# Kernel tuning notes

Hardware: AMD Instinct MI355X
Metric: run time of the kernel (lower is better)

## Reference

```python
import jax, jax.numpy as jnp
import numpy as np

N_NODES = 20000
N_EDGES = 160000
N_GRAPHS = 1000
IN_DIM = 11
HID = 128
EDGE_DIM = 3
N_LAYERS = 5
BN_EPS = 1e-5


def setup_inputs() -> dict:
    key = jax.random.key(0)
    ks = jax.random.split(key, 24)
    x = jax.random.normal(ks[0], (N_NODES, IN_DIM), dtype=jnp.float32)
    edge_index = jax.random.randint(ks[1], (2, N_EDGES), 0, N_NODES, dtype=jnp.int64)
    batch = jnp.sort(jax.random.randint(ks[2], (N_NODES,), 0, N_GRAPHS, dtype=jnp.int64))
    edge_attr = jax.random.uniform(ks[3], (N_EDGES, EDGE_DIM), dtype=jnp.float32)
    s_in = 1.0 / np.sqrt(IN_DIM)
    s_z = 1.0 / np.sqrt(2 * HID + EDGE_DIM)
    s_h = 1.0 / np.sqrt(HID)
    W_in = jax.random.uniform(ks[4], (IN_DIM, HID), minval=-s_in, maxval=s_in)
    b_in = jax.random.uniform(ks[5], (HID,), minval=-s_in, maxval=s_in)
    Wf = jax.random.uniform(ks[6], (N_LAYERS, 2 * HID + EDGE_DIM, HID), minval=-s_z, maxval=s_z)
    bf = jax.random.uniform(ks[7], (N_LAYERS, HID), minval=-s_z, maxval=s_z)
    Ws = jax.random.uniform(ks[8], (N_LAYERS, 2 * HID + EDGE_DIM, HID), minval=-s_z, maxval=s_z)
    bs = jax.random.uniform(ks[9], (N_LAYERS, HID), minval=-s_z, maxval=s_z)
    gamma = jnp.ones((N_LAYERS, HID), dtype=jnp.float32)
    beta = jnp.zeros((N_LAYERS, HID), dtype=jnp.float32)
    W1 = jax.random.uniform(ks[10], (HID, HID), minval=-s_h, maxval=s_h)
    b1 = jax.random.uniform(ks[11], (HID,), minval=-s_h, maxval=s_h)
    W2 = jax.random.uniform(ks[12], (HID, HID), minval=-s_h, maxval=s_h)
    b2 = jax.random.uniform(ks[13], (HID,), minval=-s_h, maxval=s_h)
    W3 = jax.random.uniform(ks[14], (HID, 1), minval=-s_h, maxval=s_h)
    b3 = jax.random.uniform(ks[15], (1,), minval=-s_h, maxval=s_h)
    return {"x": x, "edge_index": edge_index, "batch": batch, "edge_attr": edge_attr,
            "W_in": W_in, "b_in": b_in, "Wf": Wf, "bf": bf, "Ws": Ws, "bs": bs,
            "gamma": gamma, "beta": beta, "W1": W1, "b1": b1, "W2": W2, "b2": b2,
            "W3": W3, "b3": b3}


def reference(x, edge_index, batch, edge_attr, W_in, b_in, Wf, bf, Ws, bs,
              gamma, beta, W1, b1, W2, b2, W3, b3):
    src = edge_index[0]  # x_j (source / neighbor)
    dst = edge_index[1]  # x_i (target / aggregation index)
    # in-degree per node for mean aggregation (zero-degree -> divide by 1, yields 0)
    deg = jax.ops.segment_sum(jnp.ones((N_EDGES,), jnp.float32), dst, num_segments=N_NODES)
    deg = jnp.maximum(deg, 1.0)[:, None]

    h = x @ W_in + b_in  # [N, H]
    for l in range(N_LAYERS):
        # CGConv: z = [x_i, x_j, e]; msg = sigmoid(z Wf) * softplus(z Ws); residual + mean-aggr
        z = jnp.concatenate([h[dst], h[src], edge_attr], axis=-1)  # [E, 2H+D]
        msg = jax.nn.sigmoid(z @ Wf[l] + bf[l]) * jax.nn.softplus(z @ Ws[l] + bs[l])
        agg = jax.ops.segment_sum(msg, dst, num_segments=N_NODES) / deg
        h = h + agg
        # BatchNorm1d (training-mode batch stats, biased variance)
        mu = jnp.mean(h, axis=0)
        var = jnp.mean((h - mu) ** 2, axis=0)
        h = (h - mu) * jax.lax.rsqrt(var + BN_EPS) * gamma[l] + beta[l]
        h = jax.nn.relu(h)
        # dropout omitted (eval mode)

    # global mean pool over graphs
    cnt = jax.ops.segment_sum(jnp.ones((N_NODES,), jnp.float32), batch, num_segments=N_GRAPHS)
    g = jax.ops.segment_sum(h, batch, num_segments=N_GRAPHS) / jnp.maximum(cnt, 1.0)[:, None]

    g = jax.nn.relu(g @ W1 + b1)
    g = jax.nn.relu(g @ W2 + b2)
    return g @ W3 + b3  # [G, 1]
```

## Files before the change

kernel.cpp:

```cpp
#include <hip/hip_runtime.h>
#include <math.h>

#define NN 20000
#define NE 160000
#define NG 1000
#define IND 11
#define H 128
#define ED 3
#define NL 5
#define ZDH (259*128)
#define BN_EPSF 1e-5f
#define BPAD 17
#define EPW 16

typedef unsigned short ushort_t;
typedef unsigned int uint_t;
typedef __attribute__((ext_vector_type(8))) short bf8_t;
typedef __attribute__((ext_vector_type(4))) float f4_t;

__device__ inline ushort_t f2bf(float x) {
    unsigned int u = __float_as_uint(x);
    unsigned int r = (u + 0x7fffu + ((u >> 16) & 1u)) >> 16;
    return (ushort_t)r;
}
__device__ inline float bf2f(ushort_t b) {
    return __uint_as_float(((unsigned int)b) << 16);
}


__global__ void deg_int_kernel(const int* __restrict__ dst, int* __restrict__ degi) {
    int e = blockIdx.x * blockDim.x + threadIdx.x;
    if (e < NE) atomicAdd(&degi[dst[e]], 1);
}

__global__ __launch_bounds__(256) void reserve_kernel(const int* __restrict__ degi,
                                                      int* __restrict__ cursor,
                                                      float* __restrict__ invdeg,
                                                      int* __restrict__ counter) {
    int n = blockIdx.x * blockDim.x + threadIdx.x;
    int lane = threadIdx.x & 63;
    int v = (n < NN) ? degi[n] : 0;
    int x = v;
#pragma unroll
    for (int st = 1; st < 64; st <<= 1) {
        int y = __shfl_up(x, st, 64);
        if (lane >= st) x += y;
    }
    int total = __shfl(x, 63, 64);
    int base = 0;
    if (lane == 63) base = atomicAdd(counter, total);
    base = __shfl(base, 63, 64);
    if (n < NN) {
        cursor[n] = base + x - v;
        invdeg[n] = 1.0f / (float)(v < 1 ? 1 : v);
    }
}

__global__ void scatter_kernel(const int* __restrict__ src, const int* __restrict__ dst,
                               const float* __restrict__ ea,
                               const float* __restrict__ invdeg,
                               int* __restrict__ cursor, float4* __restrict__ csr_ea4,
                               int* __restrict__ csr_dst, float* __restrict__ csr_inv) {
    int e = blockIdx.x * blockDim.x + threadIdx.x;
    if (e < NE) {
        int d = dst[e];
        int pos = atomicAdd(&cursor[d], 1);
        float4 r;
        r.x = ea[e * ED + 0];
        r.y = ea[e * ED + 1];
        r.z = ea[e * ED + 2];
        r.w = __int_as_float(src[e]);
        csr_ea4[pos] = r;
        csr_dst[pos] = d;
        csr_inv[pos] = invdeg[d];
    }
}

__global__ void flag_kernel(const int* __restrict__ csr_dst, unsigned* __restrict__ endmask) {
    int e = blockIdx.x * blockDim.x + threadIdx.x;
    if (e < NE) {
        int d = csr_dst[e];
        int dn = (e + 1 < NE) ? csr_dst[e + 1] : -1;
        if (d != dn) atomicOr(&endmask[e >> 5], 1u << (e & 31));
    }
}

__global__ void wprep_kernel(const float* __restrict__ Wf, const float* __restrict__ Ws,
                             ushort_t* __restrict__ Wt) {
    int idx = blockIdx.x * 256 + threadIdx.x;
    if (idx >= NL * 512 * H) return;
    int k = idx & 127;
    int n = (idx >> 7) & 511;
    int l = idx >> 16;
    int t = n >> 7, j = n & 127;
    const float* W = (t == 0 || t == 2) ? Wf : Ws;
    int krow = (t < 2) ? k : (H + k);
    Wt[idx] = f2bf(W[(size_t)l * ZDH + krow * H + j]);
}


__global__ __launch_bounds__(H) void hin_kernel(const float* __restrict__ x,
                                                const float* __restrict__ Win,
                                                const float* __restrict__ bin,
                                                float* __restrict__ h) {
    int n = blockIdx.x;
    int j = threadIdx.x;
    __shared__ float xr[IND];
    if (j < IND) xr[j] = x[n * IND + j];
    __syncthreads();
    float acc = bin[j];
#pragma unroll
    for (int k = 0; k < IND; ++k) acc = fmaf(xr[k], Win[k * H + j], acc);
    h[(size_t)n * H + j] = acc;
}

__global__ __launch_bounds__(256, 2) void node_gemm_mfma(const float* __restrict__ hsrc,
                                                         float* __restrict__ hbn,
                                                         const ushort_t* __restrict__ Wt,
                                                         const float* __restrict__ sum,
                                                         const float* __restrict__ sumsq,
                                                         const float* __restrict__ gamma,
                                                         const float* __restrict__ beta,
                                                         int applyBN,
                                                         uint_t* __restrict__ ppack,
                                                         uint_t* __restrict__ qpack) {
    __shared__ __align__(16) ushort_t lbF[128 * BPAD * 8];
    __shared__ __align__(16) ushort_t lbS[128 * BPAD * 8];
    int pair = blockIdx.y;
    int wave = threadIdx.x >> 6;
    int lane = threadIdx.x & 63;
    int sub = lane & 15;
    int quad = lane >> 4;
    int m0 = blockIdx.x * 64 + wave * 16;
    int writeH = applyBN && (pair == 0);

    const ushort_t* whF = Wt + (size_t)(2 * pair) * 128 * H;
    const ushort_t* whS = Wt + (size_t)(2 * pair + 1) * 128 * H;

    for (int c = threadIdx.x; c < 2048; c += 256) {
        int n = c >> 4, k = c & 15;
        *(bf8_t*)(lbF + ((size_t)n * BPAD + k) * 8) = *(const bf8_t*)(whF + n * H + k * 8);
        *(bf8_t*)(lbS + ((size_t)n * BPAD + k) * 8) = *(const bf8_t*)(whS + n * H + k * 8);
    }

    bf8_t aHi[4], aLo[4];
    int r = m0 + sub;
    int rc = r < NN ? r : NN - 1;
#pragma unroll
    for (int ks = 0; ks < 4; ++ks) {
        int kb = ks * 32 + quad * 8;
        const float* hp = hsrc + (size_t)rc * H + kb;
        float4 v0 = *(const float4*)hp;
        float4 v1 = *(const float4*)(hp + 4);
        float vv[8] = {v0.x, v0.y, v0.z, v0.w, v1.x, v1.y, v1.z, v1.w};
        if (applyBN) {
            float4 su0 = *(const float4*)&sum[kb],   su1 = *(const float4*)&sum[kb + 4];
            float4 sq0 = *(const float4*)&sumsq[kb], sq1 = *(const float4*)&sumsq[kb + 4];
            float4 ga0 = *(const float4*)&gamma[kb], ga1 = *(const float4*)&gamma[kb + 4];
            float4 be0 = *(const float4*)&beta[kb],  be1 = *(const float4*)&beta[kb + 4];
            float su[8] = {su0.x, su0.y, su0.z, su0.w, su1.x, su1.y, su1.z, su1.w};
            float sq[8] = {sq0.x, sq0.y, sq0.z, sq0.w, sq1.x, sq1.y, sq1.z, sq1.w};
            float ga[8] = {ga0.x, ga0.y, ga0.z, ga0.w, ga1.x, ga1.y, ga1.z, ga1.w};
            float be[8] = {be0.x, be0.y, be0.z, be0.w, be1.x, be1.y, be1.z, be1.w};
#pragma unroll
            for (int i = 0; i < 8; ++i) {
                float mu  = su[i] * (1.0f / NN);
                float var = sq[i] * (1.0f / NN) - mu * mu;
                float sc  = ga[i] * rsqrtf(var + BN_EPSF);
                float sh  = be[i] - mu * sc;
                float v = fmaf(vv[i], sc, sh);
                vv[i] = v > 0.0f ? v : 0.0f;
            }
        }
        bf8_t hi8, lo8;
#pragma unroll
        for (int i = 0; i < 8; ++i) {
            ushort_t hi = f2bf(vv[i]);
            hi8[i] = (short)hi;
            lo8[i] = (short)f2bf(vv[i] - bf2f(hi));
        }
        aHi[ks] = hi8;
        aLo[ks] = lo8;
        if (writeH && r < NN) {
            float* op = hbn + (size_t)r * H + kb;
            *(float4*)op = make_float4(vv[0], vv[1], vv[2], vv[3]);
            *(float4*)(op + 4) = make_float4(vv[4], vv[5], vv[6], vv[7]);
        }
    }
    __syncthreads();

    f4_t accF[8], accS[8];
#pragma unroll
    for (int b = 0; b < 8; ++b) { accF[b] = (f4_t){0.f, 0.f, 0.f, 0.f}; accS[b] = (f4_t){0.f, 0.f, 0.f, 0.f}; }

#pragma unroll
    for (int nt = 0; nt < 8; ++nt) {
#pragma unroll
        for (int ks = 0; ks < 4; ++ks) {
            size_t lo = ((size_t)(nt * 16 + sub) * BPAD + ks * 4 + quad) * 8;
            bf8_t bF = *(const bf8_t*)(lbF + lo);
            bf8_t bS = *(const bf8_t*)(lbS + lo);
            accF[nt] = __builtin_amdgcn_mfma_f32_16x16x32_bf16(aHi[ks], bF, accF[nt], 0, 0, 0);
            accF[nt] = __builtin_amdgcn_mfma_f32_16x16x32_bf16(aLo[ks], bF, accF[nt], 0, 0, 0);
            accS[nt] = __builtin_amdgcn_mfma_f32_16x16x32_bf16(aHi[ks], bS, accS[nt], 0, 0, 0);
            accS[nt] = __builtin_amdgcn_mfma_f32_16x16x32_bf16(aLo[ks], bS, accS[nt], 0, 0, 0);
        }
    }

    uint_t* outp = pair ? qpack : ppack;
#pragma unroll
    for (int nt = 0; nt < 8; ++nt) {
        int col = nt * 16 + sub;
#pragma unroll
        for (int rr = 0; rr < 4; ++rr) {
            int row = m0 + quad * 4 + rr;
            if (row < NN) {
                uint_t lo = f2bf(accF[nt][rr]);
                uint_t hi = f2bf(accS[nt][rr]);
                outp[(size_t)row * H + col] = lo | (hi << 16);
            }
        }
    }
}

__global__ __launch_bounds__(256) void agg_edge_kernel(const int4* __restrict__ csr_fe,
                                                       const int* __restrict__ csr_dst,
                                                       const float* __restrict__ csr_inv,
                                                       const unsigned* __restrict__ endmask,
                                                       const float* __restrict__ Wf,
                                                       const float* __restrict__ bf,
                                                       const float* __restrict__ Ws,
                                                       const float* __restrict__ bs,
                                                       const uint_t* __restrict__ ppack,
                                                       const uint_t* __restrict__ qpack,
                                                       float* __restrict__ h,
                                                       float* __restrict__ sum,
                                                       float* __restrict__ sumsq) {
    int tid = threadIdx.x;
    if (blockIdx.x == 0 && tid < H) { sum[tid] = 0.0f; sumsq[tid] = 0.0f; }
    int lane = tid & 63;
    int wv = tid >> 6;
    int base = (blockIdx.x * 4 + wv) * EPW;
    int c0 = 2 * lane;

    float2 wf0 = *(const float2*)&Wf[256 * H + c0];
    float2 wf1 = *(const float2*)&Wf[257 * H + c0];
    float2 wf2 = *(const float2*)&Wf[258 * H + c0];
    float2 ws0 = *(const float2*)&Ws[256 * H + c0];
    float2 ws1 = *(const float2*)&Ws[257 * H + c0];
    float2 ws2 = *(const float2*)&Ws[258 * H + c0];
    float2 bf2_ = *(const float2*)&bf[c0];
    float2 bs2_ = *(const float2*)&bs[c0];

    int4 fe = csr_fe[base + (lane & (EPW - 1))];
    int  dd = csr_dst[base + (lane & (EPW - 1))];
    int  ivr = __float_as_int(csr_inv[base + (lane & (EPW - 1))]);
    unsigned mword = endmask[base >> 5];
    unsigned mask = __builtin_amdgcn_readfirstlane((mword >> (base & 31)) & 0xFFFFu);

    uint2 q[8];
#pragma unroll
    for (int i = 0; i < 8; ++i) {
        int s = __builtin_amdgcn_readlane(fe.w, i);
        q[i] = *(const uint2*)&qpack[(size_t)s * H + c0];
    }

    int dcur = __builtin_amdgcn_readlane(dd, 0);
    uint2 ppc = *(const uint2*)&ppack[(size_t)dcur * H + c0];
    float pf0 = __uint_as_float(ppc.x << 16), ps0 = __uint_as_float(ppc.x & 0xFFFF0000u);
    float pf1 = __uint_as_float(ppc.y << 16), ps1 = __uint_as_float(ppc.y & 0xFFFF0000u);
    unsigned m = mask;
    int e0 = m ? __builtin_ctz(m) : EPW;
    int dnext = 0;
    uint2 ppN = ppc;
    if (e0 + 1 < EPW) {
        dnext = __builtin_amdgcn_readlane(dd, e0 + 1);
        ppN = *(const uint2*)&ppack[(size_t)dnext * H + c0];
    }

    float acc0 = 0.f, acc1 = 0.f;

#pragma unroll
    for (int tb = 0; tb < EPW; tb += 8) {
#pragma unroll
        for (int i = 0; i < 8; ++i) {
            int t = tb + i;
            float ex = __int_as_float(__builtin_amdgcn_readlane(fe.x, t));
            float ey = __int_as_float(__builtin_amdgcn_readlane(fe.y, t));
            float ez = __int_as_float(__builtin_amdgcn_readlane(fe.z, t));
            uint2 qq = q[i];
            if (t + 8 < EPW) {
                int s2 = __builtin_amdgcn_readlane(fe.w, t + 8);
                q[i] = *(const uint2*)&qpack[(size_t)s2 * H + c0];
            }
            float qf0 = __uint_as_float(qq.x << 16);
            float qs0 = __uint_as_float(qq.x & 0xFFFF0000u);
            float qf1 = __uint_as_float(qq.y << 16);
            float qs1 = __uint_as_float(qq.y & 0xFFFF0000u);
            float f0 = fmaf(ex, wf0.x, fmaf(ey, wf1.x, fmaf(ez, wf2.x, pf0 + bf2_.x + qf0)));
            float v0 = fmaf(ex, ws0.x, fmaf(ey, ws1.x, fmaf(ez, ws2.x, ps0 + bs2_.x + qs0)));
            float f1 = fmaf(ex, wf0.y, fmaf(ey, wf1.y, fmaf(ez, wf2.y, pf1 + bf2_.y + qf1)));
            float v1 = fmaf(ex, ws0.y, fmaf(ey, ws1.y, fmaf(ez, ws2.y, ps1 + bs2_.y + qs1)));
            float sig0 = __builtin_amdgcn_rcpf(1.0f + __expf(-f0));
            float sp0  = fmaxf(v0, 0.0f) + __logf(1.0f + __expf(-fabsf(v0)));
            float sig1 = __builtin_amdgcn_rcpf(1.0f + __expf(-f1));
            float sp1  = fmaxf(v1, 0.0f) + __logf(1.0f + __expf(-fabsf(v1)));
            acc0 = fmaf(sig0, sp0, acc0);
            acc1 = fmaf(sig1, sp1, acc1);
            if (mask & (1u << t)) {
                float inv = __int_as_float(__builtin_amdgcn_readlane(ivr, t));
                atomicAdd(&h[(size_t)dcur * H + c0], acc0 * inv);
                atomicAdd(&h[(size_t)dcur * H + c0 + 1], acc1 * inv);
                acc0 = 0.f; acc1 = 0.f;
                dcur = dnext;
                pf0 = __uint_as_float(ppN.x << 16); ps0 = __uint_as_float(ppN.x & 0xFFFF0000u);
                pf1 = __uint_as_float(ppN.y << 16); ps1 = __uint_as_float(ppN.y & 0xFFFF0000u);
                m &= m - 1;
                int e1 = m ? __builtin_ctz(m) : EPW;
                if (e1 + 1 < EPW) {
                    dnext = __builtin_amdgcn_readlane(dd, e1 + 1);
                    ppN = *(const uint2*)&ppack[(size_t)dnext * H + c0];
                }
            }
        }
    }
    if (!(mask & (1u << (EPW - 1)))) {
        float inv = __int_as_float(__builtin_amdgcn_readlane(ivr, EPW - 1));
        atomicAdd(&h[(size_t)dcur * H + c0], acc0 * inv);
        atomicAdd(&h[(size_t)dcur * H + c0 + 1], acc1 * inv);
    }
}

__global__ __launch_bounds__(H) void stats_kernel(const float* __restrict__ h,
                                                  float* __restrict__ sum,
                                                  float* __restrict__ sumsq) {
    int j = threadIdx.x;
    float s = 0.0f, ss = 0.0f;
    int n = blockIdx.x * 8;
    for (; n + 7 < NN; n += gridDim.x * 8) {
        float v[8];
#pragma unroll
        for (int i = 0; i < 8; ++i) v[i] = h[(size_t)(n + i) * H + j];
#pragma unroll
        for (int i = 0; i < 8; ++i) { s += v[i]; ss = fmaf(v[i], v[i], ss); }
    }
    for (; n < NN; ++n) {
        float v = h[(size_t)n * H + j];
        s += v;
        ss = fmaf(v, v, ss);
    }
    atomicAdd(&sum[j], s);
    atomicAdd(&sumsq[j], ss);
}

__global__ __launch_bounds__(H) void pool_kernel(const float* __restrict__ h,
                                                 const int* __restrict__ batch,
                                                 const float* __restrict__ sum,
                                                 const float* __restrict__ sumsq,
                                                 const float* __restrict__ gamma,
                                                 const float* __restrict__ beta,
                                                 float* __restrict__ g,
                                                 float* __restrict__ cnt) {
    int j = threadIdx.x;
    float mu  = sum[j] * (1.0f / NN);
    float var = sumsq[j] * (1.0f / NN) - mu * mu;
    float sc  = gamma[j] * rsqrtf(var + BN_EPSF);
    float sh  = beta[j] - mu * sc;
    for (int n = blockIdx.x; n < NN; n += gridDim.x) {
        int b = batch[n];
        float v = fmaf(h[(size_t)n * H + j], sc, sh);
        v = v > 0.0f ? v : 0.0f;
        atomicAdd(&g[(size_t)b * H + j], v);
        if (j == 0) atomicAdd(&cnt[b], 1.0f);
    }
}

__global__ __launch_bounds__(H) void mlp_kernel(const float* __restrict__ g,
                                                const float* __restrict__ cnt,
                                                const float* __restrict__ W1,
                                                const float* __restrict__ b1,
                                                const float* __restrict__ W2,
                                                const float* __restrict__ b2,
                                                const float* __restrict__ W3,
                                                const float* __restrict__ b3,
                                                float* __restrict__ out) {
    int gid = blockIdx.x, j = threadIdx.x;
    __shared__ float s1[H];
    __shared__ float s2[H];
    __shared__ float wsum[2];
    float c = cnt[gid];
    c = c < 1.0f ? 1.0f : c;
    s1[j] = g[gid * H + j] / c;
    __syncthreads();
    float a = b1[j];
    for (int k = 0; k < H; ++k) a = fmaf(s1[k], W1[k * H + j], a);
    a = a > 0.0f ? a : 0.0f;
    s2[j] = a;
    __syncthreads();
    float t = b2[j];
    for (int k = 0; k < H; ++k) t = fmaf(s2[k], W2[k * H + j], t);
    t = t > 0.0f ? t : 0.0f;
    float p = t * W3[j];
    for (int off = 32; off > 0; off >>= 1) p += __shfl_down(p, off, 64);
    if ((j & 63) == 0) wsum[j >> 6] = p;
    __syncthreads();
    if (j == 0) out[gid] = wsum[0] + wsum[1] + b3[0];
}

extern "C" void kernel_launch(void* const* d_in, const int* in_sizes, int n_in,
                              void* d_out, int out_size, void* d_ws, size_t ws_size,
                              hipStream_t stream) {
    const float* x     = (const float*)d_in[0];
    const int*   ei    = (const int*)d_in[1];
    const int*   srcp  = ei;
    const int*   dstp  = ei + NE;
    const int*   batch = (const int*)d_in[2];
    const float* ea    = (const float*)d_in[3];
    const float* Win   = (const float*)d_in[4];
    const float* bin   = (const float*)d_in[5];
    const float* Wf    = (const float*)d_in[6];
    const float* bf    = (const float*)d_in[7];
    const float* Ws    = (const float*)d_in[8];
    const float* bs    = (const float*)d_in[9];
    const float* gamma = (const float*)d_in[10];
    const float* beta  = (const float*)d_in[11];
    const float* W1    = (const float*)d_in[12];
    const float* b1    = (const float*)d_in[13];
    const float* W2    = (const float*)d_in[14];
    const float* b2    = (const float*)d_in[15];
    const float* W3    = (const float*)d_in[16];
    const float* b3    = (const float*)d_in[17];
    float* out = (float*)d_out;

    const size_t NH = (size_t)NN * H;
    float* wsp = (float*)d_ws;
    size_t off = 0;
    float* hA     = wsp + off; off += NH;
    float* hB     = wsp + off; off += NH;
    uint_t* ppack = (uint_t*)(wsp + off); off += NH;
    uint_t* qpack = (uint_t*)(wsp + off); off += NH;
    float* invdeg = wsp + off; off += NN;
    float* sum    = wsp + off; off += H;
    float* sumsq  = wsp + off; off += H;
    float* g      = wsp + off; off += (size_t)NG * H;
    float* cnt    = wsp + off; off += NG;
    off = (off + 3) & ~(size_t)3;
    float4* csr_ea4 = (float4*)(wsp + off); off += (size_t)NE * 4;
    float* csr_inv = wsp + off; off += NE;
    int* degi      = (int*)(wsp + off); off += NN;
    int* counter   = (int*)(wsp + off); off += 1;
    unsigned* endmask = (unsigned*)(wsp + off); off += NE / 32;
    int* cursor    = (int*)(wsp + off); off += NN;
    int* csr_dst   = (int*)(wsp + off); off += NE;
    off = (off + 3) & ~(size_t)3;
    ushort_t* Wt = (ushort_t*)(wsp + off); off += (size_t)NL * 512 * H / 2;

    hipMemsetAsync(degi, 0, (NN + 1 + NE / 32) * sizeof(int), stream);
    deg_int_kernel<<<(NE + 255) / 256, 256, 0, stream>>>(dstp, degi);
    reserve_kernel<<<(NN + 255) / 256, 256, 0, stream>>>(degi, cursor, invdeg, counter);
    scatter_kernel<<<(NE + 255) / 256, 256, 0, stream>>>(srcp, dstp, ea, invdeg, cursor,
                                                         csr_ea4, csr_dst, csr_inv);
    flag_kernel<<<(NE + 255) / 256, 256, 0, stream>>>(csr_dst, endmask);
    wprep_kernel<<<(NL * 512 * H + 255) / 256, 256, 0, stream>>>(Wf, Ws, Wt);

    hin_kernel<<<NN, H, 0, stream>>>(x, Win, bin, hA);

    float* hRead = hA;
    for (int l = 0; l < NL; ++l) {
        float* hTgt = (l == 0) ? hA : ((l & 1) ? hB : hA);
        node_gemm_mfma<<<dim3((NN + 63) / 64, 2), 256, 0, stream>>>(
            hRead, hTgt,
            Wt + (size_t)l * 512 * H,
            sum, sumsq,
            gamma + (size_t)(l ? l - 1 : 0) * H,
            beta  + (size_t)(l ? l - 1 : 0) * H,
            l > 0, ppack, qpack);
        agg_edge_kernel<<<NE / (4 * EPW), 256, 0, stream>>>((const int4*)csr_ea4, csr_dst,
                                                            csr_inv, endmask,
                                                            Wf + (size_t)l * ZDH, bf + (size_t)l * H,
                                                            Ws + (size_t)l * ZDH, bs + (size_t)l * H,
                                                            ppack, qpack,
                                                            hTgt, sum, sumsq);
        stats_kernel<<<512, H, 0, stream>>>(hTgt, sum, sumsq);
        hRead = hTgt;
    }

    hipMemsetAsync(g, 0, ((size_t)NG * H + NG) * sizeof(float), stream);
    pool_kernel<<<2048, H, 0, stream>>>(hRead, batch, sum, sumsq,
                                        gamma + (size_t)(NL - 1) * H,
                                        beta + (size_t)(NL - 1) * H, g, cnt);
    mlp_kernel<<<NG, H, 0, stream>>>(g, cnt, W1, b1, W2, b2, W3, b3, out);
}
```

Before: 491.4 us.

## Fuse prep kernels and replace atomic pooling with segment-based pool+MLP kernel

Merges degree counting, weight conversion, input projection and a new graph-boundary computation into one prep launch. Uses the sorted batch array to build per-graph start offsets, so pooling reads contiguous node ranges without atomics and is fused with the MLP head, processing four graphs per block to reuse weight loads. This drops several launches and a memset, and removes atomic contention in pooling, at the cost of fewer pool blocks (250) doing sequential per-graph reductions.

```diff
diff --git a/kernel.cpp b/kernel.cpp
--- a/kernel.cpp
+++ b/kernel.cpp
@@ -12,6 +12,13 @@
 #define BN_EPSF 1e-5f
 #define BPAD 17
 #define EPW 16
+#define GP 4
+
+#define DEG_BLKS ((NE + 255) / 256)
+#define WPREP_BLKS ((NL * 512 * H + 255) / 256)
+#define GB_BLKS ((NN + 255) / 256)
+#define HIN_BLKS 512
+#define PREP_GRID (DEG_BLKS + WPREP_BLKS + GB_BLKS + HIN_BLKS)
 
 typedef unsigned short ushort_t;
 typedef unsigned int uint_t;
@@ -27,10 +34,57 @@
     return __uint_as_float(((unsigned int)b) << 16);
 }
 
-
-__global__ void deg_int_kernel(const int* __restrict__ dst, int* __restrict__ degi) {
-    int e = blockIdx.x * blockDim.x + threadIdx.x;
-    if (e < NE) atomicAdd(&degi[dst[e]], 1);
+__global__ __launch_bounds__(256) void prep_fused(const int* __restrict__ dst,
+                                                  int* __restrict__ degi,
+                                                  const float* __restrict__ Wf,
+                                                  const float* __restrict__ Ws,
+                                                  ushort_t* __restrict__ Wt,
+                                                  const float* __restrict__ x,
+                                                  const float* __restrict__ Win,
+                                                  const float* __restrict__ bin,
+                                                  float* __restrict__ h,
+                                                  const int* __restrict__ batch,
+                                                  int* __restrict__ gstart) {
+    int b = blockIdx.x;
+    int tid = threadIdx.x;
+    if (b < DEG_BLKS) {
+        int e = b * 256 + tid;
+        if (e < NE) atomicAdd(&degi[dst[e]], 1);
+    } else if (b < DEG_BLKS + WPREP_BLKS) {
+        int idx = (b - DEG_BLKS) * 256 + tid;
+        if (idx < NL * 512 * H) {
+            int k = idx & 127;
+            int n = (idx >> 7) & 511;
+            int l = idx >> 16;
+            int t = n >> 7, j = n & 127;
+            const float* W = (t == 0 || t == 2) ? Wf : Ws;
+            int krow = (t < 2) ? k : (H + k);
+            Wt[idx] = f2bf(W[(size_t)l * ZDH + krow * H + j]);
+        }
+    } else if (b < DEG_BLKS + WPREP_BLKS + GB_BLKS) {
+        int n = (b - DEG_BLKS - WPREP_BLKS) * 256 + tid;
+        if (n < NN) {
+            int b0 = batch[n];
+            int bn = (n + 1 < NN) ? batch[n + 1] : NG;
+            if (n == 0)
+                for (int t = 0; t <= b0; ++t) gstart[t] = 0;
+            for (int t = b0 + 1; t <= bn; ++t) gstart[t] = n + 1;
+        }
+    } else {
+        __shared__ float lw[IND * H];
+        for (int i = tid; i < IND * H; i += 256) lw[i] = Win[i];
+        __syncthreads();
+        int j = tid & 127;
+        float bj = bin[j];
+        int rb = b - (DEG_BLKS + WPREP_BLKS + GB_BLKS);
+        for (int n = rb * 2 + (tid >> 7); n < NN; n += HIN_BLKS * 2) {
+            const float* xr = x + (size_t)n * IND;
+            float acc = bj;
+#pragma unroll
+            for (int k = 0; k < IND; ++k) acc = fmaf(xr[k], lw[k * H + j], acc);
+            h[(size_t)n * H + j] = acc;
+        }
+    }
 }
 
 __global__ __launch_bounds__(256) void reserve_kernel(const int* __restrict__ degi,
@@ -83,35 +137,6 @@
         int dn = (e + 1 < NE) ? csr_dst[e + 1] : -1;
         if (d != dn) atomicOr(&endmask[e >> 5], 1u << (e & 31));
     }
-}
-
-__global__ void wprep_kernel(const float* __restrict__ Wf, const float* __restrict__ Ws,
-                             ushort_t* __restrict__ Wt) {
-    int idx = blockIdx.x * 256 + threadIdx.x;
-    if (idx >= NL * 512 * H) return;
-    int k = idx & 127;
-    int n = (idx >> 7) & 511;
-    int l = idx >> 16;
-    int t = n >> 7, j = n & 127;
-    const float* W = (t == 0 || t == 2) ? Wf : Ws;
-    int krow = (t < 2) ? k : (H + k);
-    Wt[idx] = f2bf(W[(size_t)l * ZDH + krow * H + j]);
-}
-
-
-__global__ __launch_bounds__(H) void hin_kernel(const float* __restrict__ x,
-                                                const float* __restrict__ Win,
-                                                const float* __restrict__ bin,
-                                                float* __restrict__ h) {
-    int n = blockIdx.x;
-    int j = threadIdx.x;
-    __shared__ float xr[IND];
-    if (j < IND) xr[j] = x[n * IND + j];
-    __syncthreads();
-    float acc = bin[j];
-#pragma unroll
-    for (int k = 0; k < IND; ++k) acc = fmaf(xr[k], Win[k * H + j], acc);
-    h[(size_t)n * H + j] = acc;
 }
 
 __global__ __launch_bounds__(256, 2) void node_gemm_mfma(const float* __restrict__ hsrc,
@@ -353,58 +378,82 @@
     atomicAdd(&sumsq[j], ss);
 }
 
-__global__ __launch_bounds__(H) void pool_kernel(const float* __restrict__ h,
-                                                 const int* __restrict__ batch,
-                                                 const float* __restrict__ sum,
-                                                 const float* __restrict__ sumsq,
-                                                 const float* __restrict__ gamma,
-                                                 const float* __restrict__ beta,
-                                                 float* __restrict__ g,
-                                                 float* __restrict__ cnt) {
+__global__ __launch_bounds__(H) void pool_mlp_kernel(const float* __restrict__ h,
+                                                     const int* __restrict__ gstart,
+                                                     const float* __restrict__ sum,
+                                                     const float* __restrict__ sumsq,
+                                                     const float* __restrict__ gamma,
+                                                     const float* __restrict__ beta,
+                                                     const float* __restrict__ W1,
+                                                     const float* __restrict__ b1,
+                                                     const float* __restrict__ W2,
+                                                     const float* __restrict__ b2,
+                                                     const float* __restrict__ W3,
+                                                     const float* __restrict__ b3,
+                                                     float* __restrict__ out) {
     int j = threadIdx.x;
     float mu  = sum[j] * (1.0f / NN);
     float var = sumsq[j] * (1.0f / NN) - mu * mu;
     float sc  = gamma[j] * rsqrtf(var + BN_EPSF);
     float sh  = beta[j] - mu * sc;
-    for (int n = blockIdx.x; n < NN; n += gridDim.x) {
-        int b = batch[n];
-        float v = fmaf(h[(size_t)n * H + j], sc, sh);
-        v = v > 0.0f ? v : 0.0f;
-        atomicAdd(&g[(size_t)b * H + j], v);
-        if (j == 0) atomicAdd(&cnt[b], 1.0f);
-    }
-}
-
-__global__ __launch_bounds__(H) void mlp_kernel(const float* __restrict__ g,
-                                                const float* __restrict__ cnt,
-                                                const float* __restrict__ W1,
-                                                const float* __restrict__ b1,
-                                                const float* __restrict__ W2,
-                                                const float* __restrict__ b2,
-                                                const float* __restrict__ W3,
-                                                const float* __restrict__ b3,
-                                                float* __restrict__ out) {
-    int gid = blockIdx.x, j = threadIdx.x;
-    __shared__ float s1[H];
-    __shared__ float s2[H];
-    __shared__ float wsum[2];
-    float c = cnt[gid];
-    c = c < 1.0f ? 1.0f : c;
-    s1[j] = g[gid * H + j] / c;
+
+    __shared__ float s1[GP][H];
+    __shared__ float s2[GP][H];
+
+#pragma unroll
+    for (int gi = 0; gi < GP; ++gi) {
+        int g0 = blockIdx.x * GP + gi;
+        int a = gstart[g0], e = gstart[g0 + 1];
+        float p0 = 0.f, p1 = 0.f, p2 = 0.f, p3 = 0.f;
+        int n = a;
+        for (; n + 3 < e; n += 4) {
+            float v0 = fmaf(h[(size_t)(n + 0) * H + j], sc, sh);
+            float v1 = fmaf(h[(size_t)(n + 1) * H + j], sc, sh);
+            float v2 = fmaf(h[(size_t)(n + 2) * H + j], sc, sh);
+            float v3 = fmaf(h[(size_t)(n + 3) * H + j], sc, sh);
+            p0 += fmaxf(v0, 0.f); p1 += fmaxf(v1, 0.f);
+            p2 += fmaxf(v2, 0.f); p3 += fmaxf(v3, 0.f);
+        }
+        for (; n < e; ++n) {
+            float v = fmaf(h[(size_t)n * H + j], sc, sh);
+            p0 += fmaxf(v, 0.f);
+        }
+        float cf = (float)(e - a);
+        if (cf < 1.f) cf = 1.f;
+        s1[gi][j] = ((p0 + p1) + (p2 + p3)) / cf;
+    }
     __syncthreads();
-    float a = b1[j];
-    for (int k = 0; k < H; ++k) a = fmaf(s1[k], W1[k * H + j], a);
-    a = a > 0.0f ? a : 0.0f;
-    s2[j] = a;
+
+    float a1[GP];
+#pragma unroll
+    for (int gi = 0; gi < GP; ++gi) a1[gi] = b1[j];
+    for (int k = 0; k < H; ++k) {
+        float w = W1[k * H + j];
+#pragma unroll
+        for (int gi = 0; gi < GP; ++gi) a1[gi] = fmaf(s1[gi][k], w, a1[gi]);
+    }
+#pragma unroll
+    for (int gi = 0; gi < GP; ++gi) s2[gi][j] = fmaxf(a1[gi], 0.f);
     __syncthreads();
-    float t = b2[j];
-    for (int k = 0; k < H; ++k) t = fmaf(s2[k], W2[k * H + j], t);
-    t = t > 0.0f ? t : 0.0f;
-    float p = t * W3[j];
-    for (int off = 32; off > 0; off >>= 1) p += __shfl_down(p, off, 64);
-    if ((j & 63) == 0) wsum[j >> 6] = p;
+
+#pragma unroll
+    for (int gi = 0; gi < GP; ++gi) a1[gi] = b2[j];
+    for (int k = 0; k < H; ++k) {
+        float w = W2[k * H + j];
+#pragma unroll
+        for (int gi = 0; gi < GP; ++gi) a1[gi] = fmaf(s2[gi][k], w, a1[gi]);
+    }
+
+    float w3 = W3[j];
+    __shared__ float wred[2][GP];
+#pragma unroll
+    for (int gi = 0; gi < GP; ++gi) {
+        float p = fmaxf(a1[gi], 0.f) * w3;
+        for (int off2 = 32; off2 > 0; off2 >>= 1) p += __shfl_down(p, off2, 64);
+        if ((j & 63) == 0) wred[j >> 6][gi] = p;
+    }
     __syncthreads();
-    if (j == 0) out[gid] = wsum[0] + wsum[1] + b3[0];
+    if (j < GP) out[blockIdx.x * GP + j] = wred[0][j] + wred[1][j] + b3[0];
 }
 
 extern "C" void kernel_launch(void* const* d_in, const int* in_sizes, int n_in,
@@ -442,8 +491,7 @@
     float* invdeg = wsp + off; off += NN;
     float* sum    = wsp + off; off += H;
     float* sumsq  = wsp + off; off += H;
-    float* g      = wsp + off; off += (size_t)NG * H;
-    float* cnt    = wsp + off; off += NG;
+    int* gstart   = (int*)(wsp + off); off += NG + 1;
     off = (off + 3) & ~(size_t)3;
     float4* csr_ea4 = (float4*)(wsp + off); off += (size_t)NE * 4;
     float* csr_inv = wsp + off; off += NE;
@@ -456,14 +504,12 @@
     ushort_t* Wt = (ushort_t*)(wsp + off); off += (size_t)NL * 512 * H / 2;
 
     hipMemsetAsync(degi, 0, (NN + 1 + NE / 32) * sizeof(int), stream);
-    deg_int_kernel<<<(NE + 255) / 256, 256, 0, stream>>>(dstp, degi);
+    prep_fused<<<PREP_GRID, 256, 0, stream>>>(dstp, degi, Wf, Ws, Wt,
+                                              x, Win, bin, hA, batch, gstart);
     reserve_kernel<<<(NN + 255) / 256, 256, 0, stream>>>(degi, cursor, invdeg, counter);
     scatter_kernel<<<(NE + 255) / 256, 256, 0, stream>>>(srcp, dstp, ea, invdeg, cursor,
                                                          csr_ea4, csr_dst, csr_inv);
     flag_kernel<<<(NE + 255) / 256, 256, 0, stream>>>(csr_dst, endmask);
-    wprep_kernel<<<(NL * 512 * H + 255) / 256, 256, 0, stream>>>(Wf, Ws, Wt);
-
-    hin_kernel<<<NN, H, 0, stream>>>(x, Win, bin, hA);
 
     float* hRead = hA;
     for (int l = 0; l < NL; ++l) {
@@ -485,9 +531,8 @@
         hRead = hTgt;
     }
 
-    hipMemsetAsync(g, 0, ((size_t)NG * H + NG) * sizeof(float), stream);
-    pool_kernel<<<2048, H, 0, stream>>>(hRead, batch, sum, sumsq,
-                                        gamma + (size_t)(NL - 1) * H,
-                                        beta + (size_t)(NL - 1) * H, g, cnt);
-    mlp_kernel<<<NG, H, 0, stream>>>(g, cnt, W1, b1, W2, b2, W3, b3, out);
-}
+    pool_mlp_kernel<<<NG / GP, H, 0, stream>>>(hRead, gstart, sum, sumsq,
+                                               gamma + (size_t)(NL - 1) * H,
+                                               beta + (size_t)(NL - 1) * H,
+                                               W1, b1, W2, b2, W3, b3, out);
+}
```

Result: faster. 475.7 us (-3.2%).
